# Performance work log

Measured on AMD Instinct MI355X. Metric: run time of the kernel, lower is better.

## Reference

```python
import jax, jax.numpy as jnp
import numpy as np

D = 1024
H = 16
HD = D // H


def setup_inputs() -> dict:
    key = jax.random.key(0)
    ks = jax.random.split(key, 9)
    s = 1.0 / np.sqrt(D)
    x = jax.random.normal(ks[0], (2, 2048, D), dtype=jnp.float32)
    Wq = jax.random.uniform(ks[1], (D, D), jnp.float32, -s, s)
    bq = jax.random.uniform(ks[2], (D,), jnp.float32, -s, s)
    Wk = jax.random.uniform(ks[3], (D, D), jnp.float32, -s, s)
    bk = jax.random.uniform(ks[4], (D,), jnp.float32, -s, s)
    Wv = jax.random.uniform(ks[5], (D, D), jnp.float32, -s, s)
    bv = jax.random.uniform(ks[6], (D,), jnp.float32, -s, s)
    Wo = jax.random.uniform(ks[7], (D, D), jnp.float32, -s, s)
    bo = jax.random.uniform(ks[8], (D,), jnp.float32, -s, s)
    return {"x": x, "Wq": Wq, "bq": bq, "Wk": Wk, "bk": bk,
            "Wv": Wv, "bv": bv, "Wo": Wo, "bo": bo}


def reference(x, Wq, bq, Wk, bk, Wv, bv, Wo, bo):
    B, S, _ = x.shape
    # project and split heads -> [B, H, S, HD]
    def split(t):
        return t.reshape(B, S, H, HD).transpose(0, 2, 1, 3)
    q = split(x @ Wq + bq)
    k = split(x @ Wk + bk)
    v = split(x @ Wv + bv)
    scores = jnp.einsum('bhqd,bhkd->bhqk', q, k) / np.sqrt(HD).astype(np.float32)
    attn = jax.nn.softmax(scores, axis=-1)
    ctx = jnp.einsum('bhqk,bhkd->bhqd', attn, v)  # [B,H,S,HD]
    ctx = ctx.transpose(0, 2, 1, 3).reshape(B, S, D)
    return ctx @ Wo + bo
```

## Files before the change

### kernel.cpp

```cpp
#include <hip/hip_runtime.h>
#include <hip/hip_bf16.h>
#include <math.h>

#define BB 2
#define SS 2048
#define DD 1024
#define HH 16
#define HD 64
#define MM (BB * SS)

typedef __bf16 bf16;
typedef __attribute__((ext_vector_type(8))) __bf16 bf16x8;
typedef __attribute__((ext_vector_type(4))) __bf16 bf16x4;
typedef __attribute__((ext_vector_type(4))) float f32x4;

__device__ __forceinline__ void glds16(const bf16* g, bf16* l) {
    __builtin_amdgcn_global_load_lds(
        (const __attribute__((address_space(1))) void*)g,
        (__attribute__((address_space(3))) void*)l, 16, 0, 0);
}

__global__ __launch_bounds__(256) void cvt_x(const float* __restrict__ x,
                                             bf16* __restrict__ xb) {
    int i = (blockIdx.x * 256 + threadIdx.x) * 4;
    float4 v = *(const float4*)(x + i);
    bf16x4 o;
    o[0] = (bf16)v.x; o[1] = (bf16)v.y; o[2] = (bf16)v.z; o[3] = (bf16)v.w;
    *(bf16x4*)(xb + i) = o;
}

__global__ __launch_bounds__(256) void cvt_w(
    const float* __restrict__ W0, const float* __restrict__ W1,
    const float* __restrict__ W2, const float* __restrict__ W3,
    bf16* __restrict__ Wt) {
    const float* W = (blockIdx.z == 0) ? W0 : (blockIdx.z == 1) ? W1
                   : (blockIdx.z == 2) ? W2 : W3;
    bf16* dst = Wt + (size_t)blockIdx.z * DD * DD;

    __shared__ float T[64][65];
    int k0 = blockIdx.y * 64, n0 = blockIdx.x * 64;
    int tr = threadIdx.x >> 4, tc = (threadIdx.x & 15) * 4;
#pragma unroll
    for (int u = 0; u < 4; u++) {
        int r = tr + u * 16;
        float4 v = *(const float4*)&W[(size_t)(k0 + r) * DD + n0 + tc];
        T[tc + 0][r] = v.x; T[tc + 1][r] = v.y;
        T[tc + 2][r] = v.z; T[tc + 3][r] = v.w;
    }
    __syncthreads();
#pragma unroll
    for (int u = 0; u < 4; u++) {
        int r = tr + u * 16;
        bf16x4 o;
        o[0] = (bf16)T[r][tc + 0]; o[1] = (bf16)T[r][tc + 1];
        o[2] = (bf16)T[r][tc + 2]; o[3] = (bf16)T[r][tc + 3];
        *(bf16x4*)&dst[(size_t)(n0 + r) * DD + k0 + tc] = o;
    }
}

__global__ __launch_bounds__(256) void vt_kernel(const bf16* __restrict__ V,
                                                 bf16* __restrict__ Vt) {
    const int bh = blockIdx.y;
    const int b = bh >> 4, h = bh & 15;
    const int s0 = blockIdx.x * 64;

    __shared__ bf16 T[64][72];
    const int r = threadIdx.x >> 2;
    const int c0 = (threadIdx.x & 3) * 16;

    const bf16* src = V + ((size_t)(b * SS + s0 + r)) * DD + h * HD + c0;
    *(bf16x8*)&T[r][c0]     = *(const bf16x8*)(src);
    *(bf16x8*)&T[r][c0 + 8] = *(const bf16x8*)(src + 8);
    __syncthreads();

    bf16x8 o0, o1;
#pragma unroll
    for (int i = 0; i < 8; i++) o0[i] = T[c0 + i][r];
#pragma unroll
    for (int i = 0; i < 8; i++) o1[i] = T[c0 + 8 + i][r];
    bf16* dst = Vt + ((size_t)bh * HD + r) * SS + s0 + c0;
    *(bf16x8*)dst       = o0;
    *(bf16x8*)(dst + 8) = o1;
}

__global__ __launch_bounds__(256) void mfma_gemm(
    const bf16* __restrict__ A, const bf16* __restrict__ Wt0,
    const float* __restrict__ b0, const float* __restrict__ b1,
    const float* __restrict__ b2,
    bf16* __restrict__ o0, bf16* __restrict__ o1, bf16* __restrict__ o2,
    float* __restrict__ ofp32) {
    const int z = blockIdx.z;
    const bf16* Wt = Wt0 + (size_t)z * DD * DD;
    const float* bias = (z == 0) ? b0 : (z == 1) ? b1 : b2;
    bf16* dstb = (z == 0) ? o0 : (z == 1) ? o1 : o2;

    __shared__ __align__(16) bf16 As[128 * 64];
    __shared__ __align__(16) bf16 Bs[128 * 64];

    const int tid = threadIdx.x;
    const int lane = tid & 63;
    const int w = tid >> 6;
    const int l15 = lane & 15, quad = lane >> 4;
    const int m0 = blockIdx.y * 128;
    const int n0 = blockIdx.x * 128;
    const int mw = (w & 1) * 64;
    const int nw = (w >> 1) * 64;

    f32x4 acc[4][4];
#pragma unroll
    for (int i = 0; i < 4; i++)
#pragma unroll
        for (int j = 0; j < 4; j++) acc[i][j] = (f32x4){0.f, 0.f, 0.f, 0.f};

    for (int kt = 0; kt < DD; kt += 64) {
        __syncthreads();
#pragma unroll
        for (int u = 0; u < 4; u++) {
            int j = tid + u * 256;
            int row = j >> 3, cp = j & 7;
            int c = cp ^ (row & 7);
            glds16(A  + (size_t)(m0 + row) * DD + kt + c * 8, &As[j * 8]);
            glds16(Wt + (size_t)(n0 + row) * DD + kt + c * 8, &Bs[j * 8]);
        }
        __syncthreads();

#pragma unroll
        for (int kh = 0; kh < 2; kh++) {
            bf16x8 af[4], bf[4];
#pragma unroll
            for (int i = 0; i < 4; i++) {
                int ra = mw + i * 16 + l15;
                int ja = ra * 8 + ((kh * 4 + quad) ^ (ra & 7));
                af[i] = *(const bf16x8*)&As[ja * 8];
                int rb = nw + i * 16 + l15;
                int jb = rb * 8 + ((kh * 4 + quad) ^ (rb & 7));
                bf[i] = *(const bf16x8*)&Bs[jb * 8];
            }
#pragma unroll
            for (int i = 0; i < 4; i++)
#pragma unroll
                for (int j = 0; j < 4; j++)
                    acc[i][j] = __builtin_amdgcn_mfma_f32_16x16x32_bf16(
                        af[i], bf[j], acc[i][j], 0, 0, 0);
        }
    }

    float bcol[4];
#pragma unroll
    for (int j = 0; j < 4; j++) bcol[j] = bias[n0 + nw + j * 16 + l15];

    if (ofp32) {
#pragma unroll
        for (int i = 0; i < 4; i++)
#pragma unroll
            for (int j = 0; j < 4; j++)
#pragma unroll
                for (int r = 0; r < 4; r++) {
                    int row = m0 + mw + i * 16 + quad * 4 + r;
                    int col = n0 + nw + j * 16 + l15;
                    ofp32[(size_t)row * DD + col] = acc[i][j][r] + bcol[j];
                }
    } else {
#pragma unroll
        for (int i = 0; i < 4; i++)
#pragma unroll
            for (int j = 0; j < 4; j++)
#pragma unroll
                for (int r = 0; r < 4; r++) {
                    int row = m0 + mw + i * 16 + quad * 4 + r;
                    int col = n0 + nw + j * 16 + l15;
                    dstb[(size_t)row * DD + col] = (bf16)(acc[i][j][r] + bcol[j]);
                }
    }
}

__global__ __launch_bounds__(256) void mfma_attn(
    const bf16* __restrict__ Qb, const bf16* __restrict__ Kb,
    const bf16* __restrict__ Vtg, bf16* __restrict__ ctxb) {
    __shared__ __align__(16) bf16 Qs[64 * 64];
    __shared__ __align__(16) bf16 Ks[64 * 64];
    __shared__ __align__(16) bf16 Vs[64 * 64];
    __shared__ __align__(16) bf16 Ps[4][16 * 64];

    const int tid = threadIdx.x;
    const int lane = tid & 63;
    const int w = tid >> 6;
    const int l15 = lane & 15, quad = lane >> 4;
    const int bh = blockIdx.y;
    const int b = bh >> 4, h = bh & 15;
    const int q0 = blockIdx.x * 64;
    const size_t mb = (size_t)b * SS;
    const int hc = h * HD;
    const bf16* Vt_bh = Vtg + (size_t)bh * HD * SS;
    bf16* Pw = &Ps[w][0];

#pragma unroll
    for (int u = 0; u < 2; u++) {
        int j = tid + u * 256;
        int row = j >> 3, cp = j & 7;
        int c = cp ^ (row & 7);
        glds16(Qb + (mb + q0 + row) * DD + hc + c * 8, &Qs[j * 8]);
    }
    __syncthreads();

    bf16x8 qf[2];
    {
        int rq = w * 16 + l15;
#pragma unroll
        for (int kh = 0; kh < 2; kh++) {
            int jq = rq * 8 + ((kh * 4 + quad) ^ (rq & 7));
            qf[kh] = *(const bf16x8*)&Qs[jq * 8];
        }
    }

    float l_cur = 0.0f;
    f32x4 o[4];
#pragma unroll
    for (int nb = 0; nb < 4; nb++) o[nb] = (f32x4){0.f, 0.f, 0.f, 0.f};

    const float SCL = 0.18033688011112042f;

    int pw_off[4];
#pragma unroll
    for (int kb = 0; kb < 4; kb++) {
        int cw = kb * 2 + (quad >> 1);
        pw_off[kb] = l15 * 64 + ((cw ^ (l15 & 7)) << 3) + (quad & 1) * 4;
    }

    for (int kt = 0; kt < SS; kt += 64) {
        __syncthreads();
#pragma unroll
        for (int u = 0; u < 2; u++) {
            int j = tid + u * 256;
            int row = j >> 3, cp = j & 7;
            int c = cp ^ (row & 7);
            glds16(Kb + (mb + kt + row) * DD + hc + c * 8, &Ks[j * 8]);
            glds16(Vt_bh + (size_t)row * SS + kt + c * 8, &Vs[j * 8]);
        }
        __syncthreads();

        f32x4 sc[4];
#pragma unroll
        for (int kb = 0; kb < 4; kb++) sc[kb] = (f32x4){0.f, 0.f, 0.f, 0.f};
#pragma unroll
        for (int kb = 0; kb < 4; kb++) {
            int rk = kb * 16 + l15;
#pragma unroll
            for (int kh = 0; kh < 2; kh++) {
                int jk = rk * 8 + ((kh * 4 + quad) ^ (rk & 7));
                bf16x8 kf = *(const bf16x8*)&Ks[jk * 8];
                sc[kb] = __builtin_amdgcn_mfma_f32_16x16x32_bf16(
                    kf, qf[kh], sc[kb], 0, 0, 0);
            }
        }

        float rsum = 0.f;
#pragma unroll
        for (int kb = 0; kb < 4; kb++) {
            bf16x4 pvec;
#pragma unroll
            for (int r = 0; r < 4; r++) {
                float p = exp2f(sc[kb][r] * SCL);
                rsum += p;
                pvec[r] = (bf16)p;
            }
            *(bf16x4*)&Pw[pw_off[kb]] = pvec;
        }
        rsum += __shfl_xor(rsum, 16, 64);
        rsum += __shfl_xor(rsum, 32, 64);
        l_cur += rsum;

#pragma unroll
        for (int kh = 0; kh < 2; kh++) {
            bf16x8 pf = *(const bf16x8*)&Pw[l15 * 64 + (((kh * 4 + quad) ^ (l15 & 7)) << 3)];
#pragma unroll
            for (int nb = 0; nb < 4; nb++) {
                int rv = nb * 16 + l15;
                int jv = rv * 8 + ((kh * 4 + quad) ^ (rv & 7));
                bf16x8 vf = *(const bf16x8*)&Vs[jv * 8];
                o[nb] = __builtin_amdgcn_mfma_f32_16x16x32_bf16(
                    pf, vf, o[nb], 0, 0, 0);
            }
        }
    }

    float linv = 1.0f / l_cur;
    float li[4];
#pragma unroll
    for (int r = 0; r < 4; r++) li[r] = __shfl(linv, quad * 4 + r, 64);
#pragma unroll
    for (int nb = 0; nb < 4; nb++)
#pragma unroll
        for (int r = 0; r < 4; r++) {
            int qrow = q0 + w * 16 + quad * 4 + r;
            ctxb[(mb + qrow) * DD + hc + nb * 16 + l15] = (bf16)(o[nb][r] * li[r]);
        }
}

extern "C" void kernel_launch(void* const* d_in, const int* in_sizes, int n_in,
                              void* d_out, int out_size, void* d_ws, size_t ws_size,
                              hipStream_t stream) {
    const float* x  = (const float*)d_in[0];
    const float* Wq = (const float*)d_in[1];
    const float* bq = (const float*)d_in[2];
    const float* Wk = (const float*)d_in[3];
    const float* bk = (const float*)d_in[4];
    const float* Wv = (const float*)d_in[5];
    const float* bv = (const float*)d_in[6];
    const float* Wo = (const float*)d_in[7];
    const float* bo = (const float*)d_in[8];
    float* out = (float*)d_out;

    char* base = (char*)d_ws;
    bf16* xb   = (bf16*)(base);
    bf16* Wt   = (bf16*)(base + (8ull  << 20));
    bf16* Qb   = (bf16*)(base + (16ull << 20));
    bf16* Kb   = (bf16*)(base + (24ull << 20));
    bf16* Vb   = (bf16*)(base + (32ull << 20));
    bf16* ctxb = (bf16*)(base + (40ull << 20));
    bf16* Vtg  = xb;

    cvt_x<<<dim3((MM * DD) / (256 * 4)), dim3(256), 0, stream>>>(x, xb);
    cvt_w<<<dim3(16, 16, 4), dim3(256), 0, stream>>>(Wq, Wk, Wv, Wo, Wt);

    mfma_gemm<<<dim3(DD / 128, MM / 128, 3), dim3(256), 0, stream>>>(
        xb, Wt, bq, bk, bv, Qb, Kb, Vb, nullptr);

    vt_kernel<<<dim3(SS / 64, BB * HH), dim3(256), 0, stream>>>(Vb, Vtg);

    mfma_attn<<<dim3(SS / 64, BB * HH), dim3(256), 0, stream>>>(Qb, Kb, Vtg, ctxb);

    mfma_gemm<<<dim3(DD / 128, MM / 128, 1), dim3(256), 0, stream>>>(
        ctxb, Wt + 3ull * DD * DD, bo, bo, bo, nullptr, nullptr, nullptr, out);
}
```

Before: 229.8 us.

## Process 128 query rows per attention block to reuse K/V tiles

Each attention workgroup now handles 128 queries instead of 64, with every wave computing two 16-row query groups against the same K and V tiles in shared memory. V fragments are loaded once per k-step and reused for both groups, halving global K/V traffic and LDS V reads per query. The cost is double the accumulator registers and P buffer space, and half as many workgroups (512), which may reduce occupancy and latency hiding on the GPU.

```diff
diff --git a/kernel.cpp b/kernel.cpp
--- a/kernel.cpp
+++ b/kernel.cpp
@@ -177,10 +177,10 @@
 __global__ __launch_bounds__(256) void mfma_attn(
     const bf16* __restrict__ Qb, const bf16* __restrict__ Kb,
     const bf16* __restrict__ Vtg, bf16* __restrict__ ctxb) {
-    __shared__ __align__(16) bf16 Qs[64 * 64];
+    __shared__ __align__(16) bf16 Qs[128 * 64];
     __shared__ __align__(16) bf16 Ks[64 * 64];
     __shared__ __align__(16) bf16 Vs[64 * 64];
-    __shared__ __align__(16) bf16 Ps[4][16 * 64];
+    __shared__ __align__(16) bf16 Ps[4][32 * 64];
 
     const int tid = threadIdx.x;
     const int lane = tid & 63;
@@ -188,14 +188,14 @@
     const int l15 = lane & 15, quad = lane >> 4;
     const int bh = blockIdx.y;
     const int b = bh >> 4, h = bh & 15;
-    const int q0 = blockIdx.x * 64;
+    const int q0 = blockIdx.x * 128;
     const size_t mb = (size_t)b * SS;
     const int hc = h * HD;
     const bf16* Vt_bh = Vtg + (size_t)bh * HD * SS;
     bf16* Pw = &Ps[w][0];
 
 #pragma unroll
-    for (int u = 0; u < 2; u++) {
+    for (int u = 0; u < 4; u++) {
         int j = tid + u * 256;
         int row = j >> 3, cp = j & 7;
         int c = cp ^ (row & 7);
@@ -203,20 +203,23 @@
     }
     __syncthreads();
 
-    bf16x8 qf[2];
-    {
-        int rq = w * 16 + l15;
+    bf16x8 qf[2][2];
+#pragma unroll
+    for (int g = 0; g < 2; g++) {
+        int rq = w * 32 + g * 16 + l15;
 #pragma unroll
         for (int kh = 0; kh < 2; kh++) {
             int jq = rq * 8 + ((kh * 4 + quad) ^ (rq & 7));
-            qf[kh] = *(const bf16x8*)&Qs[jq * 8];
-        }
-    }
-
-    float l_cur = 0.0f;
-    f32x4 o[4];
-#pragma unroll
-    for (int nb = 0; nb < 4; nb++) o[nb] = (f32x4){0.f, 0.f, 0.f, 0.f};
+            qf[g][kh] = *(const bf16x8*)&Qs[jq * 8];
+        }
+    }
+
+    float l_cur[2] = {0.0f, 0.0f};
+    f32x4 o[2][4];
+#pragma unroll
+    for (int g = 0; g < 2; g++)
+#pragma unroll
+        for (int nb = 0; nb < 4; nb++) o[g][nb] = (f32x4){0.f, 0.f, 0.f, 0.f};
 
     const float SCL = 0.18033688011112042f;
 
@@ -239,62 +242,75 @@
         }
         __syncthreads();
 
-        f32x4 sc[4];
-#pragma unroll
-        for (int kb = 0; kb < 4; kb++) sc[kb] = (f32x4){0.f, 0.f, 0.f, 0.f};
-#pragma unroll
-        for (int kb = 0; kb < 4; kb++) {
-            int rk = kb * 16 + l15;
-#pragma unroll
-            for (int kh = 0; kh < 2; kh++) {
-                int jk = rk * 8 + ((kh * 4 + quad) ^ (rk & 7));
-                bf16x8 kf = *(const bf16x8*)&Ks[jk * 8];
-                sc[kb] = __builtin_amdgcn_mfma_f32_16x16x32_bf16(
-                    kf, qf[kh], sc[kb], 0, 0, 0);
-            }
-        }
-
-        float rsum = 0.f;
-#pragma unroll
-        for (int kb = 0; kb < 4; kb++) {
-            bf16x4 pvec;
-#pragma unroll
-            for (int r = 0; r < 4; r++) {
-                float p = exp2f(sc[kb][r] * SCL);
-                rsum += p;
-                pvec[r] = (bf16)p;
-            }
-            *(bf16x4*)&Pw[pw_off[kb]] = pvec;
-        }
-        rsum += __shfl_xor(rsum, 16, 64);
-        rsum += __shfl_xor(rsum, 32, 64);
-        l_cur += rsum;
+#pragma unroll
+        for (int g = 0; g < 2; g++) {
+            f32x4 sc[4];
+#pragma unroll
+            for (int kb = 0; kb < 4; kb++) sc[kb] = (f32x4){0.f, 0.f, 0.f, 0.f};
+#pragma unroll
+            for (int kb = 0; kb < 4; kb++) {
+                int rk = kb * 16 + l15;
+#pragma unroll
+                for (int kh = 0; kh < 2; kh++) {
+                    int jk = rk * 8 + ((kh * 4 + quad) ^ (rk & 7));
+                    bf16x8 kf = *(const bf16x8*)&Ks[jk * 8];
+                    sc[kb] = __builtin_amdgcn_mfma_f32_16x16x32_bf16(
+                        kf, qf[g][kh], sc[kb], 0, 0, 0);
+                }
+            }
+            float rsum = 0.f;
+#pragma unroll
+            for (int kb = 0; kb < 4; kb++) {
+                bf16x4 pvec;
+#pragma unroll
+                for (int r = 0; r < 4; r++) {
+                    float p = exp2f(sc[kb][r] * SCL);
+                    rsum += p;
+                    pvec[r] = (bf16)p;
+                }
+                *(bf16x4*)&Pw[g * (16 * 64) + pw_off[kb]] = pvec;
+            }
+            rsum += __shfl_xor(rsum, 16, 64);
+            rsum += __shfl_xor(rsum, 32, 64);
+            l_cur[g] += rsum;
+        }
 
 #pragma unroll
         for (int kh = 0; kh < 2; kh++) {
-            bf16x8 pf = *(const bf16x8*)&Pw[l15 * 64 + (((kh * 4 + quad) ^ (l15 & 7)) << 3)];
+            bf16x8 vf[4];
 #pragma unroll
             for (int nb = 0; nb < 4; nb++) {
                 int rv = nb * 16 + l15;
                 int jv = rv * 8 + ((kh * 4 + quad) ^ (rv & 7));
-                bf16x8 vf = *(const bf16x8*)&Vs[jv * 8];
-                o[nb] = __builtin_amdgcn_mfma_f32_16x16x32_bf16(
-                    pf, vf, o[nb], 0, 0, 0);
-            }
-        }
-    }
-
-    float linv = 1.0f / l_cur;
-    float li[4];
-#pragma unroll
-    for (int r = 0; r < 4; r++) li[r] = __shfl(linv, quad * 4 + r, 64);
-#pragma unroll
-    for (int nb = 0; nb < 4; nb++)
-#pragma unroll
-        for (int r = 0; r < 4; r++) {
-            int qrow = q0 + w * 16 + quad * 4 + r;
-            ctxb[(mb + qrow) * DD + hc + nb * 16 + l15] = (bf16)(o[nb][r] * li[r]);
-        }
+                vf[nb] = *(const bf16x8*)&Vs[jv * 8];
+            }
+#pragma unroll
+            for (int g = 0; g < 2; g++) {
+                bf16x8 pf = *(const bf16x8*)&Pw[g * (16 * 64) + l15 * 64 +
+                                                (((kh * 4 + quad) ^ (l15 & 7)) << 3)];
+#pragma unroll
+                for (int nb = 0; nb < 4; nb++)
+                    o[g][nb] = __builtin_amdgcn_mfma_f32_16x16x32_bf16(
+                        pf, vf[nb], o[g][nb], 0, 0, 0);
+            }
+        }
+    }
+
+#pragma unroll
+    for (int g = 0; g < 2; g++) {
+        float linv = 1.0f / l_cur[g];
+        float li[4];
+#pragma unroll
+        for (int r = 0; r < 4; r++) li[r] = __shfl(linv, quad * 4 + r, 64);
+#pragma unroll
+        for (int nb = 0; nb < 4; nb++)
+#pragma unroll
+            for (int r = 0; r < 4; r++) {
+                int qrow = q0 + w * 32 + g * 16 + quad * 4 + r;
+                ctxb[(mb + qrow) * DD + hc + nb * 16 + l15] =
+                    (bf16)(o[g][nb][r] * li[r]);
+            }
+    }
 }
 
 extern "C" void kernel_launch(void* const* d_in, const int* in_sizes, int n_in,
@@ -328,7 +344,7 @@
 
     vt_kernel<<<dim3(SS / 64, BB * HH), dim3(256), 0, stream>>>(Vb, Vtg);
 
-    mfma_attn<<<dim3(SS / 64, BB * HH), dim3(256), 0, stream>>>(Qb, Kb, Vtg, ctxb);
+    mfma_attn<<<dim3(SS / 128, BB * HH), dim3(256), 0, stream>>>(Qb, Kb, Vtg, ctxb);
 
     mfma_gemm<<<dim3(DD / 128, MM / 128, 1), dim3(256), 0, stream>>>(
         ctxb, Wt + 3ull * DD * DD, bo, bo, bo, nullptr, nullptr, nullptr, out);
```

After: 239.8 us. 4.3% more time.

## Fuse V transpose and Q scaling into projection GEMM epilogue

Applied to the files above, without the earlier changes.

The V-projection GEMM now writes its output directly in transposed [B, D, S] layout, which removes the separate vt_kernel launch and its extra read/write of V. The MFMA operand roles are swapped so each lane holds 4 consecutive output columns, letting the Q/K/out epilogues use vectorized bf16x4/float4 stores and float4 bias loads. The softmax scale (including log2e) is folded into Q at the projection, which removes one multiply per score in the attention loop. The transposed V stores are scalar bf16 writes strided by SS, so they are uncoalesced. Q is also rounded to bf16 after scaling, which slightly changes numerics.

```diff
diff --git a/kernel.cpp b/kernel.cpp
--- a/kernel.cpp
+++ b/kernel.cpp
@@ -13,6 +13,8 @@
 typedef __attribute__((ext_vector_type(8))) __bf16 bf16x8;
 typedef __attribute__((ext_vector_type(4))) __bf16 bf16x4;
 typedef __attribute__((ext_vector_type(4))) float f32x4;
+
+#define QSCL 0.18033688011112042f
 
 __device__ __forceinline__ void glds16(const bf16* g, bf16* l) {
     __builtin_amdgcn_global_load_lds(
@@ -58,41 +60,15 @@
     }
 }
 
-__global__ __launch_bounds__(256) void vt_kernel(const bf16* __restrict__ V,
-                                                 bf16* __restrict__ Vt) {
-    const int bh = blockIdx.y;
-    const int b = bh >> 4, h = bh & 15;
-    const int s0 = blockIdx.x * 64;
-
-    __shared__ bf16 T[64][72];
-    const int r = threadIdx.x >> 2;
-    const int c0 = (threadIdx.x & 3) * 16;
-
-    const bf16* src = V + ((size_t)(b * SS + s0 + r)) * DD + h * HD + c0;
-    *(bf16x8*)&T[r][c0]     = *(const bf16x8*)(src);
-    *(bf16x8*)&T[r][c0 + 8] = *(const bf16x8*)(src + 8);
-    __syncthreads();
-
-    bf16x8 o0, o1;
-#pragma unroll
-    for (int i = 0; i < 8; i++) o0[i] = T[c0 + i][r];
-#pragma unroll
-    for (int i = 0; i < 8; i++) o1[i] = T[c0 + 8 + i][r];
-    bf16* dst = Vt + ((size_t)bh * HD + r) * SS + s0 + c0;
-    *(bf16x8*)dst       = o0;
-    *(bf16x8*)(dst + 8) = o1;
-}
-
 __global__ __launch_bounds__(256) void mfma_gemm(
     const bf16* __restrict__ A, const bf16* __restrict__ Wt0,
     const float* __restrict__ b0, const float* __restrict__ b1,
     const float* __restrict__ b2,
-    bf16* __restrict__ o0, bf16* __restrict__ o1, bf16* __restrict__ o2,
+    bf16* __restrict__ Qb, bf16* __restrict__ Kb, bf16* __restrict__ Vtg,
     float* __restrict__ ofp32) {
     const int z = blockIdx.z;
     const bf16* Wt = Wt0 + (size_t)z * DD * DD;
     const float* bias = (z == 0) ? b0 : (z == 1) ? b1 : b2;
-    bf16* dstb = (z == 0) ? o0 : (z == 1) ? o1 : o2;
 
     __shared__ __align__(16) bf16 As[128 * 64];
     __shared__ __align__(16) bf16 Bs[128 * 64];
@@ -126,51 +102,77 @@
 
 #pragma unroll
         for (int kh = 0; kh < 2; kh++) {
-            bf16x8 af[4], bf[4];
+            bf16x8 wf[4], xf[4];
 #pragma unroll
             for (int i = 0; i < 4; i++) {
+                int rb = nw + i * 16 + l15;
+                int jb = rb * 8 + ((kh * 4 + quad) ^ (rb & 7));
+                wf[i] = *(const bf16x8*)&Bs[jb * 8];
                 int ra = mw + i * 16 + l15;
                 int ja = ra * 8 + ((kh * 4 + quad) ^ (ra & 7));
-                af[i] = *(const bf16x8*)&As[ja * 8];
-                int rb = nw + i * 16 + l15;
-                int jb = rb * 8 + ((kh * 4 + quad) ^ (rb & 7));
-                bf[i] = *(const bf16x8*)&Bs[jb * 8];
+                xf[i] = *(const bf16x8*)&As[ja * 8];
             }
 #pragma unroll
             for (int i = 0; i < 4; i++)
 #pragma unroll
                 for (int j = 0; j < 4; j++)
                     acc[i][j] = __builtin_amdgcn_mfma_f32_16x16x32_bf16(
-                        af[i], bf[j], acc[i][j], 0, 0, 0);
-        }
-    }
-
-    float bcol[4];
-#pragma unroll
-    for (int j = 0; j < 4; j++) bcol[j] = bias[n0 + nw + j * 16 + l15];
+                        wf[i], xf[j], acc[i][j], 0, 0, 0);
+        }
+    }
 
     if (ofp32) {
 #pragma unroll
-        for (int i = 0; i < 4; i++)
-#pragma unroll
-            for (int j = 0; j < 4; j++)
+        for (int i = 0; i < 4; i++) {
+            int nb4 = n0 + nw + i * 16 + quad * 4;
+            float4 b4 = *(const float4*)&bias[nb4];
+#pragma unroll
+            for (int j = 0; j < 4; j++) {
+                int m = m0 + mw + j * 16 + l15;
+                float4 o;
+                o.x = acc[i][j][0] + b4.x;
+                o.y = acc[i][j][1] + b4.y;
+                o.z = acc[i][j][2] + b4.z;
+                o.w = acc[i][j][3] + b4.w;
+                *(float4*)&ofp32[(size_t)m * DD + nb4] = o;
+            }
+        }
+    } else if (z == 2) {
+#pragma unroll
+        for (int i = 0; i < 4; i++) {
+            int nb4 = n0 + nw + i * 16 + quad * 4;
+            float4 b4f = *(const float4*)&bias[nb4];
+            float b4[4] = {b4f.x, b4f.y, b4f.z, b4f.w};
+#pragma unroll
+            for (int j = 0; j < 4; j++) {
+                int m = m0 + mw + j * 16 + l15;
+                int bb = m >> 11, s = m & (SS - 1);
 #pragma unroll
                 for (int r = 0; r < 4; r++) {
-                    int row = m0 + mw + i * 16 + quad * 4 + r;
-                    int col = n0 + nw + j * 16 + l15;
-                    ofp32[(size_t)row * DD + col] = acc[i][j][r] + bcol[j];
+                    int dg = nb4 + r;
+                    Vtg[((size_t)bb * 1024 + dg) * SS + s] =
+                        (bf16)(acc[i][j][r] + b4[r]);
                 }
+            }
+        }
     } else {
-#pragma unroll
-        for (int i = 0; i < 4; i++)
-#pragma unroll
-            for (int j = 0; j < 4; j++)
-#pragma unroll
-                for (int r = 0; r < 4; r++) {
-                    int row = m0 + mw + i * 16 + quad * 4 + r;
-                    int col = n0 + nw + j * 16 + l15;
-                    dstb[(size_t)row * DD + col] = (bf16)(acc[i][j][r] + bcol[j]);
-                }
+        bf16* dst = (z == 0) ? Qb : Kb;
+        const float scl = (z == 0) ? QSCL : 1.0f;
+#pragma unroll
+        for (int i = 0; i < 4; i++) {
+            int nb4 = n0 + nw + i * 16 + quad * 4;
+            float4 b4 = *(const float4*)&bias[nb4];
+#pragma unroll
+            for (int j = 0; j < 4; j++) {
+                int m = m0 + mw + j * 16 + l15;
+                bf16x4 o;
+                o[0] = (bf16)((acc[i][j][0] + b4.x) * scl);
+                o[1] = (bf16)((acc[i][j][1] + b4.y) * scl);
+                o[2] = (bf16)((acc[i][j][2] + b4.z) * scl);
+                o[3] = (bf16)((acc[i][j][3] + b4.w) * scl);
+                *(bf16x4*)&dst[(size_t)m * DD + nb4] = o;
+            }
+        }
     }
 }
 
@@ -218,8 +220,6 @@
 #pragma unroll
     for (int nb = 0; nb < 4; nb++) o[nb] = (f32x4){0.f, 0.f, 0.f, 0.f};
 
-    const float SCL = 0.18033688011112042f;
-
     int pw_off[4];
 #pragma unroll
     for (int kb = 0; kb < 4; kb++) {
@@ -260,7 +260,7 @@
             bf16x4 pvec;
 #pragma unroll
             for (int r = 0; r < 4; r++) {
-                float p = exp2f(sc[kb][r] * SCL);
+                float p = exp2f(sc[kb][r]);
                 rsum += p;
                 pvec[r] = (bf16)p;
             }
@@ -316,17 +316,14 @@
     bf16* Wt   = (bf16*)(base + (8ull  << 20));
     bf16* Qb   = (bf16*)(base + (16ull << 20));
     bf16* Kb   = (bf16*)(base + (24ull << 20));
-    bf16* Vb   = (bf16*)(base + (32ull << 20));
+    bf16* Vtg  = (bf16*)(base + (32ull << 20));
     bf16* ctxb = (bf16*)(base + (40ull << 20));
-    bf16* Vtg  = xb;
 
     cvt_x<<<dim3((MM * DD) / (256 * 4)), dim3(256), 0, stream>>>(x, xb);
     cvt_w<<<dim3(16, 16, 4), dim3(256), 0, stream>>>(Wq, Wk, Wv, Wo, Wt);
 
     mfma_gemm<<<dim3(DD / 128, MM / 128, 3), dim3(256), 0, stream>>>(
-        xb, Wt, bq, bk, bv, Qb, Kb, Vb, nullptr);
-
-    vt_kernel<<<dim3(SS / 64, BB * HH), dim3(256), 0, stream>>>(Vb, Vtg);
+        xb, Wt, bq, bk, bv, Qb, Kb, Vtg, nullptr);
 
     mfma_attn<<<dim3(SS / 64, BB * HH), dim3(256), 0, stream>>>(Qb, Kb, Vtg, ctxb);
 
```

Result: slower. 243.4 us (+5.9%).

## Split attention keys across waves and fold softmax scale into Q projection

Applied to the files above, without the earlier changes.

The attention kernel now has each of the four waves handle all 64 queries over a quarter of the key range (split-K). K and V are read straight from global memory into registers instead of being staged in LDS behind per-tile barriers. Partial outputs and row sums are reduced through LDS at the end, and the softmax scale is folded into the Q projection epilogue so the inner loop skips a multiply. The kernel also gets an occupancy hint of three blocks per unit. The risks are more register pressure from the 16 output accumulators per lane, uncoalesced direct global loads of K and V, and a serialized four-step reduction at the end.

```diff
diff --git a/kernel.cpp b/kernel.cpp
--- a/kernel.cpp
+++ b/kernel.cpp
@@ -13,6 +13,8 @@
 typedef __attribute__((ext_vector_type(8))) __bf16 bf16x8;
 typedef __attribute__((ext_vector_type(4))) __bf16 bf16x4;
 typedef __attribute__((ext_vector_type(4))) float f32x4;
+
+#define QSCL 0.18033688011112042f
 
 __device__ __forceinline__ void glds16(const bf16* g, bf16* l) {
     __builtin_amdgcn_global_load_lds(
@@ -93,6 +95,7 @@
     const bf16* Wt = Wt0 + (size_t)z * DD * DD;
     const float* bias = (z == 0) ? b0 : (z == 1) ? b1 : b2;
     bf16* dstb = (z == 0) ? o0 : (z == 1) ? o1 : o2;
+    const float scl = (z == 0 && !ofp32) ? QSCL : 1.0f;
 
     __shared__ __align__(16) bf16 As[128 * 64];
     __shared__ __align__(16) bf16 Bs[128 * 64];
@@ -169,18 +172,17 @@
                 for (int r = 0; r < 4; r++) {
                     int row = m0 + mw + i * 16 + quad * 4 + r;
                     int col = n0 + nw + j * 16 + l15;
-                    dstb[(size_t)row * DD + col] = (bf16)(acc[i][j][r] + bcol[j]);
+                    dstb[(size_t)row * DD + col] =
+                        (bf16)((acc[i][j][r] + bcol[j]) * scl);
                 }
     }
 }
 
-__global__ __launch_bounds__(256) void mfma_attn(
+__global__ __launch_bounds__(256, 3) void mfma_attn(
     const bf16* __restrict__ Qb, const bf16* __restrict__ Kb,
     const bf16* __restrict__ Vtg, bf16* __restrict__ ctxb) {
-    __shared__ __align__(16) bf16 Qs[64 * 64];
-    __shared__ __align__(16) bf16 Ks[64 * 64];
-    __shared__ __align__(16) bf16 Vs[64 * 64];
-    __shared__ __align__(16) bf16 Ps[4][16 * 64];
+    __shared__ __align__(16) bf16 Ps[4][64 * 64];
+    __shared__ float ls[4][64];
 
     const int tid = threadIdx.x;
     const int lane = tid & 63;
@@ -194,107 +196,117 @@
     const bf16* Vt_bh = Vtg + (size_t)bh * HD * SS;
     bf16* Pw = &Ps[w][0];
 
-#pragma unroll
-    for (int u = 0; u < 2; u++) {
-        int j = tid + u * 256;
-        int row = j >> 3, cp = j & 7;
-        int c = cp ^ (row & 7);
-        glds16(Qb + (mb + q0 + row) * DD + hc + c * 8, &Qs[j * 8]);
+    bf16x8 qf[4][2];
+#pragma unroll
+    for (int g = 0; g < 4; g++)
+#pragma unroll
+        for (int kh = 0; kh < 2; kh++)
+            qf[g][kh] = *(const bf16x8*)&Qb[(mb + q0 + g * 16 + l15) * DD +
+                                            hc + kh * 32 + quad * 8];
+
+    float l_part[4] = {0.f, 0.f, 0.f, 0.f};
+    f32x4 o[4][4];
+#pragma unroll
+    for (int g = 0; g < 4; g++)
+#pragma unroll
+        for (int nb = 0; nb < 4; nb++) o[g][nb] = (f32x4){0.f, 0.f, 0.f, 0.f};
+
+    const int k0w = w * (SS / 4);
+
+    for (int t = 0; t < (SS / 4) / 64; t++) {
+        const int kt = k0w + t * 64;
+
+#pragma unroll
+        for (int kb = 0; kb < 4; kb++) {
+            f32x4 sc[4];
+#pragma unroll
+            for (int g = 0; g < 4; g++) sc[g] = (f32x4){0.f, 0.f, 0.f, 0.f};
+#pragma unroll
+            for (int kh = 0; kh < 2; kh++) {
+                bf16x8 kf = *(const bf16x8*)&Kb[(mb + kt + kb * 16 + l15) * DD +
+                                                hc + kh * 32 + quad * 8];
+#pragma unroll
+                for (int g = 0; g < 4; g++)
+                    sc[g] = __builtin_amdgcn_mfma_f32_16x16x32_bf16(
+                        kf, qf[g][kh], sc[g], 0, 0, 0);
+            }
+            int cw = ((kb * 2 + (quad >> 1)) ^ (l15 & 7)) * 8 + (quad & 1) * 4;
+#pragma unroll
+            for (int g = 0; g < 4; g++) {
+                bf16x4 pvec;
+                float rs = 0.f;
+#pragma unroll
+                for (int r = 0; r < 4; r++) {
+                    float p = exp2f(sc[g][r]);
+                    rs += p;
+                    pvec[r] = (bf16)p;
+                }
+                l_part[g] += rs;
+                *(bf16x4*)&Pw[(g * 16 + l15) * 64 + cw] = pvec;
+            }
+        }
+
+#pragma unroll
+        for (int kh = 0; kh < 2; kh++) {
+            bf16x8 vf[4];
+#pragma unroll
+            for (int nb = 0; nb < 4; nb++)
+                vf[nb] = *(const bf16x8*)&Vt_bh[(size_t)(nb * 16 + l15) * SS +
+                                                kt + kh * 32 + quad * 8];
+            int cp = ((kh * 4 + quad) ^ (l15 & 7)) * 8;
+#pragma unroll
+            for (int g = 0; g < 4; g++) {
+                bf16x8 pf = *(const bf16x8*)&Pw[(g * 16 + l15) * 64 + cp];
+#pragma unroll
+                for (int nb = 0; nb < 4; nb++)
+                    o[g][nb] = __builtin_amdgcn_mfma_f32_16x16x32_bf16(
+                        pf, vf[nb], o[g][nb], 0, 0, 0);
+            }
+        }
+    }
+
+#pragma unroll
+    for (int g = 0; g < 4; g++) {
+        l_part[g] += __shfl_xor(l_part[g], 16, 64);
+        l_part[g] += __shfl_xor(l_part[g], 32, 64);
+    }
+    if (lane < 16) {
+#pragma unroll
+        for (int g = 0; g < 4; g++) ls[w][g * 16 + lane] = l_part[g];
     }
     __syncthreads();
 
-    bf16x8 qf[2];
+    float* Os = (float*)&Ps[0][0];
+#pragma unroll
+    for (int ww = 0; ww < 4; ww++) {
+        if (w == ww) {
+#pragma unroll
+            for (int g = 0; g < 4; g++)
+#pragma unroll
+                for (int nb = 0; nb < 4; nb++)
+#pragma unroll
+                    for (int r = 0; r < 4; r++) {
+                        int q = g * 16 + quad * 4 + r;
+                        int d = nb * 16 + l15;
+                        if (ww == 0) Os[q * 68 + d] = o[g][nb][r];
+                        else         Os[q * 68 + d] += o[g][nb][r];
+                    }
+        }
+        __syncthreads();
+    }
+
     {
-        int rq = w * 16 + l15;
-#pragma unroll
-        for (int kh = 0; kh < 2; kh++) {
-            int jq = rq * 8 + ((kh * 4 + quad) ^ (rq & 7));
-            qf[kh] = *(const bf16x8*)&Qs[jq * 8];
-        }
-    }
-
-    float l_cur = 0.0f;
-    f32x4 o[4];
-#pragma unroll
-    for (int nb = 0; nb < 4; nb++) o[nb] = (f32x4){0.f, 0.f, 0.f, 0.f};
-
-    const float SCL = 0.18033688011112042f;
-
-    int pw_off[4];
-#pragma unroll
-    for (int kb = 0; kb < 4; kb++) {
-        int cw = kb * 2 + (quad >> 1);
-        pw_off[kb] = l15 * 64 + ((cw ^ (l15 & 7)) << 3) + (quad & 1) * 4;
-    }
-
-    for (int kt = 0; kt < SS; kt += 64) {
-        __syncthreads();
-#pragma unroll
-        for (int u = 0; u < 2; u++) {
-            int j = tid + u * 256;
-            int row = j >> 3, cp = j & 7;
-            int c = cp ^ (row & 7);
-            glds16(Kb + (mb + kt + row) * DD + hc + c * 8, &Ks[j * 8]);
-            glds16(Vt_bh + (size_t)row * SS + kt + c * 8, &Vs[j * 8]);
-        }
-        __syncthreads();
-
-        f32x4 sc[4];
-#pragma unroll
-        for (int kb = 0; kb < 4; kb++) sc[kb] = (f32x4){0.f, 0.f, 0.f, 0.f};
-#pragma unroll
-        for (int kb = 0; kb < 4; kb++) {
-            int rk = kb * 16 + l15;
-#pragma unroll
-            for (int kh = 0; kh < 2; kh++) {
-                int jk = rk * 8 + ((kh * 4 + quad) ^ (rk & 7));
-                bf16x8 kf = *(const bf16x8*)&Ks[jk * 8];
-                sc[kb] = __builtin_amdgcn_mfma_f32_16x16x32_bf16(
-                    kf, qf[kh], sc[kb], 0, 0, 0);
-            }
-        }
-
-        float rsum = 0.f;
-#pragma unroll
-        for (int kb = 0; kb < 4; kb++) {
-            bf16x4 pvec;
-#pragma unroll
-            for (int r = 0; r < 4; r++) {
-                float p = exp2f(sc[kb][r] * SCL);
-                rsum += p;
-                pvec[r] = (bf16)p;
-            }
-            *(bf16x4*)&Pw[pw_off[kb]] = pvec;
-        }
-        rsum += __shfl_xor(rsum, 16, 64);
-        rsum += __shfl_xor(rsum, 32, 64);
-        l_cur += rsum;
-
-#pragma unroll
-        for (int kh = 0; kh < 2; kh++) {
-            bf16x8 pf = *(const bf16x8*)&Pw[l15 * 64 + (((kh * 4 + quad) ^ (l15 & 7)) << 3)];
-#pragma unroll
-            for (int nb = 0; nb < 4; nb++) {
-                int rv = nb * 16 + l15;
-                int jv = rv * 8 + ((kh * 4 + quad) ^ (rv & 7));
-                bf16x8 vf = *(const bf16x8*)&Vs[jv * 8];
-                o[nb] = __builtin_amdgcn_mfma_f32_16x16x32_bf16(
-                    pf, vf, o[nb], 0, 0, 0);
-            }
-        }
-    }
-
-    float linv = 1.0f / l_cur;
-    float li[4];
-#pragma unroll
-    for (int r = 0; r < 4; r++) li[r] = __shfl(linv, quad * 4 + r, 64);
-#pragma unroll
-    for (int nb = 0; nb < 4; nb++)
-#pragma unroll
-        for (int r = 0; r < 4; r++) {
-            int qrow = q0 + w * 16 + quad * 4 + r;
-            ctxb[(mb + qrow) * DD + hc + nb * 16 + l15] = (bf16)(o[nb][r] * li[r]);
-        }
+        int q = tid >> 2, d0 = (tid & 3) * 16;
+        float linv = 1.0f / (ls[0][q] + ls[1][q] + ls[2][q] + ls[3][q]);
+        bf16x8 oa, ob;
+#pragma unroll
+        for (int i = 0; i < 8; i++) oa[i] = (bf16)(Os[q * 68 + d0 + i] * linv);
+#pragma unroll
+        for (int i = 0; i < 8; i++) ob[i] = (bf16)(Os[q * 68 + d0 + 8 + i] * linv);
+        bf16* dst = &ctxb[(mb + q0 + q) * DD + hc + d0];
+        *(bf16x8*)dst       = oa;
+        *(bf16x8*)(dst + 8) = ob;
+    }
 }
 
 extern "C" void kernel_launch(void* const* d_in, const int* in_sizes, int n_in,
```

Result: slower. 292.0 us (+27.0%).
